# Optimization experiments

Hardware: AMD Instinct MI355X
Metric: run time of the kernel (lower is better)

Reference implementation:

```python
import jax, jax.numpy as jnp
import numpy as np

N = 40000   # number of points
K = 32      # neighbors per point (fixed-degree CSR for synthetic indices)
C = 256     # embed_dim
H = 8       # num_heads
HD = C // H # head_dim = 32
M = N * K   # number of (query, key) pairs


def setup_inputs() -> dict:
    key = jax.random.key(0)
    ks = jax.random.split(key, 12)
    s = 1.0 / np.sqrt(C).astype(np.float32)
    query_feats = jax.random.normal(ks[0], (N, C), jnp.float32)
    Wq = jax.random.normal(ks[1], (C, C), jnp.float32) * s
    bq = jax.random.normal(ks[2], (C,), jnp.float32) * 0.01
    Wk = jax.random.normal(ks[3], (C, C), jnp.float32) * s
    bk = jax.random.normal(ks[4], (C,), jnp.float32) * 0.01
    Wv = jax.random.normal(ks[5], (C, C), jnp.float32) * s
    bv = jax.random.normal(ks[6], (C,), jnp.float32) * 0.01
    Wp = jax.random.normal(ks[7], (C, C), jnp.float32) * s
    bp = jax.random.normal(ks[8], (C,), jnp.float32) * 0.01
    # CSR pair lists: index_0 sorted (K pairs per query point), index_1 = neighbor ids
    index_0 = jnp.repeat(jnp.arange(N, dtype=jnp.int32), K)
    index_1 = jax.random.randint(ks[9], (M,), 0, N, dtype=jnp.int32)
    sort_idx = jax.random.permutation(ks[10], N).astype(jnp.int32)
    return dict(query_feats=query_feats, Wq=Wq, bq=bq, Wk=Wk, bk=bk, Wv=Wv, bv=bv,
                Wp=Wp, bp=bp, index_0=index_0, index_1=index_1, sort_idx=sort_idx)


def reference(query_feats, Wq, bq, Wk, bk, Wv, bv, Wp, bp, index_0, index_1, sort_idx):
    # pe_type='none', attntion_type='qkv', key=value=query (self-attention), dropout=0
    scale = HD ** -0.5
    q = ((query_feats @ Wq) + bq).reshape(N, H, HD) * scale
    k = ((query_feats @ Wk) + bk).reshape(N, H, HD)
    v = ((query_feats @ Wv) + bv).reshape(N, H, HD)
    # sort into window-contiguous order
    qs = q[sort_idx]
    ks_ = k[sort_idx]
    vs = v[sort_idx]
    # attention_step1: per-pair QK dot over head_dim -> (M, H)
    attn = jnp.einsum('mhd,mhd->mh', qs[index_0], ks_[index_1])
    # scatter_softmax_csr over variable-length neighbor segments (grouped by index_0)
    seg_max = jax.ops.segment_max(attn, index_0, num_segments=N, indices_are_sorted=True)
    e = jnp.exp(attn - seg_max[index_0])
    seg_sum = jax.ops.segment_sum(e, index_0, num_segments=N, indices_are_sorted=True)
    p = e / seg_sum[index_0]  # (M, H)
    # attention_step2: weighted value gather + segment reduce -> (N, H, HD)
    xs = jax.ops.segment_sum(p[:, :, None] * vs[index_1], index_0,
                             num_segments=N, indices_are_sorted=True)
    # scatter back to original order: out[sort_idx] = xs
    x = jnp.zeros((N, C), query_feats.dtype).at[sort_idx].set(xs.reshape(N, C))
    # output projection
    return x @ Wp + bp
```

## Files before the change

### kernel.cpp

```cpp
#include <hip/hip_runtime.h>
#include <hip/hip_bf16.h>

#define NPTS 40000
#define KNBR 32
#define CDIM 256
#define NH 8
#define HD 32

static constexpr float QK_SCALE = 0.17677669529663687f;

typedef __attribute__((ext_vector_type(8))) __bf16 bf16x8;
typedef __attribute__((ext_vector_type(4))) __bf16 bf16x4;
typedef __attribute__((ext_vector_type(4))) float f32x4;

static __device__ __forceinline__ unsigned short bfbits(float f) {
    __bf16 h = (__bf16)f;
    union { __bf16 b; unsigned short u; } c; c.b = h;
    return c.u;
}

__global__ __launch_bounds__(256) void wtr_kernel(
    const float* __restrict__ W0, const float* __restrict__ W1,
    const float* __restrict__ W2, const float* __restrict__ W3,
    __bf16* __restrict__ T0, __bf16* __restrict__ T1,
    __bf16* __restrict__ T2, __bf16* __restrict__ T3)
{
    __shared__ float tile[32][33];
    const float* Ws[4] = {W0, W1, W2, W3};
    __bf16* Ts[4] = {T0, T1, T2, T3};
    const float* W = Ws[blockIdx.z];
    __bf16* Wt = Ts[blockIdx.z];
    const int t = threadIdx.x;
    const int k0 = blockIdx.x * 32, n0 = blockIdx.y * 32;
    const int r = t >> 3, c4 = (t & 7) * 4;
    const float4 v = *reinterpret_cast<const float4*>(&W[(k0 + r) * CDIM + n0 + c4]);
    tile[r][c4 + 0] = v.x; tile[r][c4 + 1] = v.y;
    tile[r][c4 + 2] = v.z; tile[r][c4 + 3] = v.w;
    __syncthreads();
    __bf16 o[4];
    #pragma unroll
    for (int i = 0; i < 4; ++i) o[i] = (__bf16)tile[c4 + i][r];
    *reinterpret_cast<ulong1*>(&Wt[(n0 + r) * CDIM + k0 + c4]) =
        *reinterpret_cast<ulong1*>(o);
}

__global__ __launch_bounds__(256, 2) void qkv_kernel(
    const float* __restrict__ X, const int* __restrict__ sort_idx,
    const __bf16* __restrict__ WtQ, const __bf16* __restrict__ WtK, const __bf16* __restrict__ WtV,
    const float* __restrict__ bq, const float* __restrict__ bk, const float* __restrict__ bv,
    __bf16* __restrict__ qs, unsigned int* __restrict__ kvs)
{
    __shared__ __bf16 xb[32][272];
    const int t = threadIdx.x;
    const int row0 = blockIdx.x * 32;

    #pragma unroll 8
    for (int r = 0; r < 32; ++r) {
        const int src = sort_idx[row0 + r];
        xb[r][t] = (__bf16)X[(size_t)src * CDIM + t];
    }
    __syncthreads();

    const int w = t >> 6, l = t & 63;
    const int lr = l & 15;
    const int lk = (l >> 4) * 8;
    const int nbase = w * 64;
    const __bf16* Wts[3] = {WtQ, WtK, WtV};

    f32x4 acc[3][2][4];
    #pragma unroll
    for (int s = 0; s < 3; ++s)
        #pragma unroll
        for (int mf = 0; mf < 2; ++mf)
            #pragma unroll
            for (int nf = 0; nf < 4; ++nf)
                acc[s][mf][nf] = (f32x4){0.f, 0.f, 0.f, 0.f};

    #pragma unroll 2
    for (int k0 = 0; k0 < CDIM; k0 += 32) {
        const bf16x8 a0 = *reinterpret_cast<const bf16x8*>(&xb[lr][k0 + lk]);
        const bf16x8 a1 = *reinterpret_cast<const bf16x8*>(&xb[16 + lr][k0 + lk]);
        #pragma unroll
        for (int s = 0; s < 3; ++s) {
            #pragma unroll
            for (int nf = 0; nf < 4; ++nf) {
                const bf16x8 b = *reinterpret_cast<const bf16x8*>(
                    Wts[s] + (size_t)(nbase + nf * 16 + lr) * CDIM + k0 + lk);
                acc[s][0][nf] = __builtin_amdgcn_mfma_f32_16x16x32_bf16(a0, b, acc[s][0][nf], 0, 0, 0);
                acc[s][1][nf] = __builtin_amdgcn_mfma_f32_16x16x32_bf16(a1, b, acc[s][1][nf], 0, 0, 0);
            }
        }
    }

    const int rbase = (l >> 4) * 4;
    #pragma unroll
    for (int nf = 0; nf < 4; ++nf) {
        const int col = nbase + nf * 16 + lr;
        const float bqv = bq[col], bkv = bk[col], bvv = bv[col];
        #pragma unroll
        for (int mf = 0; mf < 2; ++mf) {
            #pragma unroll
            for (int i = 0; i < 4; ++i) {
                const int row = row0 + mf * 16 + rbase + i;
                qs[row * CDIM + col] = (__bf16)((acc[0][mf][nf][i] + bqv) * QK_SCALE);
                const unsigned int kb = bfbits(acc[1][mf][nf][i] + bkv);
                const unsigned int vb = bfbits(acc[2][mf][nf][i] + bvv);
                kvs[row * CDIM + col] = kb | (vb << 16);
            }
        }
    }
}

__global__ __launch_bounds__(256, 8) void attn_kernel(
    const __bf16* __restrict__ qs, const unsigned int* __restrict__ kvs,
    const int* __restrict__ index_1, const int* __restrict__ sort_idx,
    __bf16* __restrict__ xbuf)
{
    const int wv = __builtin_amdgcn_readfirstlane(threadIdx.x) >> 6;
    const int n = blockIdx.x * 4 + wv;
    const int l = threadIdx.x & 63;
    const int c0 = l * 4;

    const bf16x4 qv4 = *reinterpret_cast<const bf16x4*>(&qs[(size_t)n * CDIM + c0]);
    const float qx = (float)qv4[0], qy = (float)qv4[1];
    const float qz = (float)qv4[2], qw = (float)qv4[3];
    float lsum = 0.f;
    float o0 = 0.f, o1 = 0.f, o2 = 0.f, o3 = 0.f;
    const int* idx = index_1 + (size_t)n * KNBR;

    #pragma unroll 4
    for (int j = 0; j < KNBR; ++j) {
        const int nb = idx[j];
        const uint4 kv = *reinterpret_cast<const uint4*>(&kvs[(size_t)nb * CDIM + c0]);
        const float k0 = __uint_as_float(kv.x << 16);
        const float v0 = __uint_as_float(kv.x & 0xffff0000u);
        const float k1 = __uint_as_float(kv.y << 16);
        const float v1 = __uint_as_float(kv.y & 0xffff0000u);
        const float k2 = __uint_as_float(kv.z << 16);
        const float v2 = __uint_as_float(kv.z & 0xffff0000u);
        const float k3 = __uint_as_float(kv.w << 16);
        const float v3 = __uint_as_float(kv.w & 0xffff0000u);
        float dot = qx * k0;
        dot = fmaf(qy, k1, dot);
        dot = fmaf(qz, k2, dot);
        dot = fmaf(qw, k3, dot);
        dot += __shfl_xor(dot, 1);
        dot += __shfl_xor(dot, 2);
        dot += __shfl_xor(dot, 4);
        const float e = __expf(dot);
        lsum += e;
        o0 = fmaf(e, v0, o0);
        o1 = fmaf(e, v1, o1);
        o2 = fmaf(e, v2, o2);
        o3 = fmaf(e, v3, o3);
    }

    const float inv = 1.f / lsum;
    const int orig = sort_idx[n];
    __bf16 o[4];
    o[0] = (__bf16)(o0 * inv); o[1] = (__bf16)(o1 * inv);
    o[2] = (__bf16)(o2 * inv); o[3] = (__bf16)(o3 * inv);
    *reinterpret_cast<ulong1*>(&xbuf[(size_t)orig * CDIM + c0]) =
        *reinterpret_cast<ulong1*>(o);
}

__global__ __launch_bounds__(256, 2) void proj_kernel(
    const __bf16* __restrict__ X, const __bf16* __restrict__ WtP, const float* __restrict__ bp,
    float* __restrict__ out)
{
    const int t = threadIdx.x;
    const int w = t >> 6, l = t & 63;
    const int row0 = blockIdx.x * 32;
    const int lr = l & 15;
    const int lk = (l >> 4) * 8;
    const int nbase = w * 64;

    const __bf16* pA0 = X + (size_t)(row0 + lr) * CDIM + lk;
    const __bf16* pA1 = X + (size_t)(row0 + 16 + lr) * CDIM + lk;

    f32x4 acc[2][4];
    #pragma unroll
    for (int mf = 0; mf < 2; ++mf)
        #pragma unroll
        for (int nf = 0; nf < 4; ++nf)
            acc[mf][nf] = (f32x4){0.f, 0.f, 0.f, 0.f};

    #pragma unroll 2
    for (int k0 = 0; k0 < CDIM; k0 += 32) {
        const bf16x8 a0 = *reinterpret_cast<const bf16x8*>(pA0 + k0);
        const bf16x8 a1 = *reinterpret_cast<const bf16x8*>(pA1 + k0);
        #pragma unroll
        for (int nf = 0; nf < 4; ++nf) {
            const bf16x8 b = *reinterpret_cast<const bf16x8*>(
                WtP + (size_t)(nbase + nf * 16 + lr) * CDIM + k0 + lk);
            acc[0][nf] = __builtin_amdgcn_mfma_f32_16x16x32_bf16(a0, b, acc[0][nf], 0, 0, 0);
            acc[1][nf] = __builtin_amdgcn_mfma_f32_16x16x32_bf16(a1, b, acc[1][nf], 0, 0, 0);
        }
    }

    const int rbase = (l >> 4) * 4;
    #pragma unroll
    for (int nf = 0; nf < 4; ++nf) {
        const int col = nbase + nf * 16 + lr;
        const float bpv = bp[col];
        #pragma unroll
        for (int mf = 0; mf < 2; ++mf) {
            #pragma unroll
            for (int i = 0; i < 4; ++i) {
                const int row = row0 + mf * 16 + rbase + i;
                out[row * CDIM + col] = acc[mf][nf][i] + bpv;
            }
        }
    }
}

extern "C" void kernel_launch(void* const* d_in, const int* in_sizes, int n_in,
                              void* d_out, int out_size, void* d_ws, size_t ws_size,
                              hipStream_t stream) {
    const float* qf  = (const float*)d_in[0];
    const float* Wq  = (const float*)d_in[1];
    const float* bq  = (const float*)d_in[2];
    const float* Wk  = (const float*)d_in[3];
    const float* bk  = (const float*)d_in[4];
    const float* Wv  = (const float*)d_in[5];
    const float* bv  = (const float*)d_in[6];
    const float* Wp  = (const float*)d_in[7];
    const float* bp  = (const float*)d_in[8];
    const int* index_1  = (const int*)d_in[10];
    const int* sort_idx = (const int*)d_in[11];
    float* out = (float*)d_out;

    __bf16* qs = (__bf16*)d_ws;
    unsigned int* kvs = (unsigned int*)(qs + (size_t)NPTS * CDIM);
    __bf16* xbuf = (__bf16*)(kvs + (size_t)NPTS * CDIM);
    __bf16* WtQ = xbuf + (size_t)NPTS * CDIM;
    __bf16* WtK = WtQ + CDIM * CDIM;
    __bf16* WtV = WtK + CDIM * CDIM;
    __bf16* WtP = WtV + CDIM * CDIM;

    wtr_kernel<<<dim3(8, 8, 4), 256, 0, stream>>>(Wq, Wk, Wv, Wp, WtQ, WtK, WtV, WtP);
    qkv_kernel<<<NPTS / 32, 256, 0, stream>>>(qf, sort_idx, WtQ, WtK, WtV, bq, bk, bv, qs, kvs);
    attn_kernel<<<NPTS / 4, 256, 0, stream>>>(qs, kvs, index_1, sort_idx, xbuf);
    proj_kernel<<<NPTS / 32, 256, 0, stream>>>(xbuf, WtP, bp, out);
}
```

Before: 289.0 us.

## Split K/V buffers, sort neighbor indices, and enlarge GEMM row tiles

Stores K and V in separate bf16 arrays instead of an interleaved packed buffer, so the attention kernel issues two 8-byte gathers per neighbor. Each wave loads its 32 neighbor indices once and bitonic-sorts them in registers, then broadcasts them with shuffles, aiming for better cache locality on the gathers. The QKV and projection GEMMs now use 64-row tiles, processing Q, K and V one after another to reuse the A fragments across more MFMAs. The risks are more memory transactions per neighbor, the cost of the sort network, and higher register pressure in the larger GEMM tiles.

Result: slower. 321.5 us (+11.3%).

```diff
diff --git a/kernel.cpp b/kernel.cpp
--- a/kernel.cpp
+++ b/kernel.cpp
@@ -12,12 +12,6 @@
 typedef __attribute__((ext_vector_type(8))) __bf16 bf16x8;
 typedef __attribute__((ext_vector_type(4))) __bf16 bf16x4;
 typedef __attribute__((ext_vector_type(4))) float f32x4;
-
-static __device__ __forceinline__ unsigned short bfbits(float f) {
-    __bf16 h = (__bf16)f;
-    union { __bf16 b; unsigned short u; } c; c.b = h;
-    return c.u;
-}
 
 __global__ __launch_bounds__(256) void wtr_kernel(
     const float* __restrict__ W0, const float* __restrict__ W1,
@@ -48,14 +42,14 @@
     const float* __restrict__ X, const int* __restrict__ sort_idx,
     const __bf16* __restrict__ WtQ, const __bf16* __restrict__ WtK, const __bf16* __restrict__ WtV,
     const float* __restrict__ bq, const float* __restrict__ bk, const float* __restrict__ bv,
-    __bf16* __restrict__ qs, unsigned int* __restrict__ kvs)
-{
-    __shared__ __bf16 xb[32][272];
+    __bf16* __restrict__ qs, __bf16* __restrict__ ksp, __bf16* __restrict__ vsp)
+{
+    __shared__ __bf16 xb[64][272];
     const int t = threadIdx.x;
-    const int row0 = blockIdx.x * 32;
+    const int row0 = blockIdx.x * 64;
 
     #pragma unroll 8
-    for (int r = 0; r < 32; ++r) {
+    for (int r = 0; r < 64; ++r) {
         const int src = sort_idx[row0 + r];
         xb[r][t] = (__bf16)X[(size_t)src * CDIM + t];
     }
@@ -65,54 +59,56 @@
     const int lr = l & 15;
     const int lk = (l >> 4) * 8;
     const int nbase = w * 64;
+    const int rbase = (l >> 4) * 4;
     const __bf16* Wts[3] = {WtQ, WtK, WtV};
-
-    f32x4 acc[3][2][4];
-    #pragma unroll
-    for (int s = 0; s < 3; ++s)
-        #pragma unroll
-        for (int mf = 0; mf < 2; ++mf)
+    const float* bias[3] = {bq, bk, bv};
+    __bf16* outs[3] = {qs, ksp, vsp};
+
+    #pragma unroll
+    for (int s = 0; s < 3; ++s) {
+        f32x4 acc[4][4];
+        #pragma unroll
+        for (int mf = 0; mf < 4; ++mf)
             #pragma unroll
             for (int nf = 0; nf < 4; ++nf)
-                acc[s][mf][nf] = (f32x4){0.f, 0.f, 0.f, 0.f};
-
-    #pragma unroll 2
-    for (int k0 = 0; k0 < CDIM; k0 += 32) {
-        const bf16x8 a0 = *reinterpret_cast<const bf16x8*>(&xb[lr][k0 + lk]);
-        const bf16x8 a1 = *reinterpret_cast<const bf16x8*>(&xb[16 + lr][k0 + lk]);
-        #pragma unroll
-        for (int s = 0; s < 3; ++s) {
+                acc[mf][nf] = (f32x4){0.f, 0.f, 0.f, 0.f};
+
+        #pragma unroll 2
+        for (int k0 = 0; k0 < CDIM; k0 += 32) {
+            bf16x8 a[4];
+            #pragma unroll
+            for (int mf = 0; mf < 4; ++mf)
+                a[mf] = *reinterpret_cast<const bf16x8*>(&xb[mf * 16 + lr][k0 + lk]);
             #pragma unroll
             for (int nf = 0; nf < 4; ++nf) {
                 const bf16x8 b = *reinterpret_cast<const bf16x8*>(
                     Wts[s] + (size_t)(nbase + nf * 16 + lr) * CDIM + k0 + lk);
-                acc[s][0][nf] = __builtin_amdgcn_mfma_f32_16x16x32_bf16(a0, b, acc[s][0][nf], 0, 0, 0);
-                acc[s][1][nf] = __builtin_amdgcn_mfma_f32_16x16x32_bf16(a1, b, acc[s][1][nf], 0, 0, 0);
+                #pragma unroll
+                for (int mf = 0; mf < 4; ++mf)
+                    acc[mf][nf] = __builtin_amdgcn_mfma_f32_16x16x32_bf16(a[mf], b, acc[mf][nf], 0, 0, 0);
             }
         }
-    }
-
-    const int rbase = (l >> 4) * 4;
-    #pragma unroll
-    for (int nf = 0; nf < 4; ++nf) {
-        const int col = nbase + nf * 16 + lr;
-        const float bqv = bq[col], bkv = bk[col], bvv = bv[col];
-        #pragma unroll
-        for (int mf = 0; mf < 2; ++mf) {
-            #pragma unroll
-            for (int i = 0; i < 4; ++i) {
-                const int row = row0 + mf * 16 + rbase + i;
-                qs[row * CDIM + col] = (__bf16)((acc[0][mf][nf][i] + bqv) * QK_SCALE);
-                const unsigned int kb = bfbits(acc[1][mf][nf][i] + bkv);
-                const unsigned int vb = bfbits(acc[2][mf][nf][i] + bvv);
-                kvs[row * CDIM + col] = kb | (vb << 16);
+
+        __bf16* const dst = outs[s];
+        #pragma unroll
+        for (int nf = 0; nf < 4; ++nf) {
+            const int col = nbase + nf * 16 + lr;
+            const float bb = bias[s][col];
+            #pragma unroll
+            for (int mf = 0; mf < 4; ++mf) {
+                #pragma unroll
+                for (int i = 0; i < 4; ++i) {
+                    const int row = row0 + mf * 16 + rbase + i;
+                    const float val = acc[mf][nf][i] + bb;
+                    dst[(size_t)row * CDIM + col] = (__bf16)(s == 0 ? val * QK_SCALE : val);
+                }
             }
         }
     }
 }
 
 __global__ __launch_bounds__(256, 8) void attn_kernel(
-    const __bf16* __restrict__ qs, const unsigned int* __restrict__ kvs,
+    const __bf16* __restrict__ qs, const __bf16* __restrict__ ksp, const __bf16* __restrict__ vsp,
     const int* __restrict__ index_1, const int* __restrict__ sort_idx,
     __bf16* __restrict__ xbuf)
 {
@@ -120,26 +116,37 @@
     const int n = blockIdx.x * 4 + wv;
     const int l = threadIdx.x & 63;
     const int c0 = l * 4;
+
+    int key = index_1[(size_t)n * KNBR + (l & 31)];
+    #pragma unroll
+    for (int k = 2; k <= 32; k <<= 1) {
+        #pragma unroll
+        for (int s = k >> 1; s > 0; s >>= 1) {
+            const int ll = l & 31;
+            const int other = __shfl_xor(key, s);
+            const bool asc = (ll & k) == 0;
+            const bool lower = (ll & s) == 0;
+            const int mn = key < other ? key : other;
+            const int mx = key < other ? other : key;
+            key = (asc == lower) ? mn : mx;
+        }
+    }
 
     const bf16x4 qv4 = *reinterpret_cast<const bf16x4*>(&qs[(size_t)n * CDIM + c0]);
     const float qx = (float)qv4[0], qy = (float)qv4[1];
     const float qz = (float)qv4[2], qw = (float)qv4[3];
     float lsum = 0.f;
     float o0 = 0.f, o1 = 0.f, o2 = 0.f, o3 = 0.f;
-    const int* idx = index_1 + (size_t)n * KNBR;
-
-    #pragma unroll 4
+
+    #pragma unroll
     for (int j = 0; j < KNBR; ++j) {
-        const int nb = idx[j];
-        const uint4 kv = *reinterpret_cast<const uint4*>(&kvs[(size_t)nb * CDIM + c0]);
-        const float k0 = __uint_as_float(kv.x << 16);
-        const float v0 = __uint_as_float(kv.x & 0xffff0000u);
-        const float k1 = __uint_as_float(kv.y << 16);
-        const float v1 = __uint_as_float(kv.y & 0xffff0000u);
-        const float k2 = __uint_as_float(kv.z << 16);
-        const float v2 = __uint_as_float(kv.z & 0xffff0000u);
-        const float k3 = __uint_as_float(kv.w << 16);
-        const float v3 = __uint_as_float(kv.w & 0xffff0000u);
+        const int nb = __shfl(key, j);
+        const uint2 kk = *reinterpret_cast<const uint2*>(&ksp[(size_t)nb * CDIM + c0]);
+        const uint2 vv = *reinterpret_cast<const uint2*>(&vsp[(size_t)nb * CDIM + c0]);
+        const float k0 = __uint_as_float(kk.x << 16);
+        const float k1 = __uint_as_float(kk.x & 0xffff0000u);
+        const float k2 = __uint_as_float(kk.y << 16);
+        const float k3 = __uint_as_float(kk.y & 0xffff0000u);
         float dot = qx * k0;
         dot = fmaf(qy, k1, dot);
         dot = fmaf(qz, k2, dot);
@@ -148,6 +155,10 @@
         dot += __shfl_xor(dot, 2);
         dot += __shfl_xor(dot, 4);
         const float e = __expf(dot);
+        const float v0 = __uint_as_float(vv.x << 16);
+        const float v1 = __uint_as_float(vv.x & 0xffff0000u);
+        const float v2 = __uint_as_float(vv.y << 16);
+        const float v3 = __uint_as_float(vv.y & 0xffff0000u);
         lsum += e;
         o0 = fmaf(e, v0, o0);
         o1 = fmaf(e, v1, o1);
@@ -170,45 +181,50 @@
 {
     const int t = threadIdx.x;
     const int w = t >> 6, l = t & 63;
-    const int row0 = blockIdx.x * 32;
+    const int row0 = blockIdx.x * 64;
     const int lr = l & 15;
     const int lk = (l >> 4) * 8;
     const int nbase = w * 64;
-
-    const __bf16* pA0 = X + (size_t)(row0 + lr) * CDIM + lk;
-    const __bf16* pA1 = X + (size_t)(row0 + 16 + lr) * CDIM + lk;
-
-    f32x4 acc[2][4];
-    #pragma unroll
-    for (int mf = 0; mf < 2; ++mf)
+    const int rbase = (l >> 4) * 4;
+
+    const __bf16* pA[4];
+    #pragma unroll
+    for (int mf = 0; mf < 4; ++mf)
+        pA[mf] = X + (size_t)(row0 + mf * 16 + lr) * CDIM + lk;
+
+    f32x4 acc[4][4];
+    #pragma unroll
+    for (int mf = 0; mf < 4; ++mf)
         #pragma unroll
         for (int nf = 0; nf < 4; ++nf)
             acc[mf][nf] = (f32x4){0.f, 0.f, 0.f, 0.f};
 
     #pragma unroll 2
     for (int k0 = 0; k0 < CDIM; k0 += 32) {
-        const bf16x8 a0 = *reinterpret_cast<const bf16x8*>(pA0 + k0);
-        const bf16x8 a1 = *reinterpret_cast<const bf16x8*>(pA1 + k0);
+        bf16x8 a[4];
+        #pragma unroll
+        for (int mf = 0; mf < 4; ++mf)
+            a[mf] = *reinterpret_cast<const bf16x8*>(pA[mf] + k0);
         #pragma unroll
         for (int nf = 0; nf < 4; ++nf) {
             const bf16x8 b = *reinterpret_cast<const bf16x8*>(
                 WtP + (size_t)(nbase + nf * 16 + lr) * CDIM + k0 + lk);
-            acc[0][nf] = __builtin_amdgcn_mfma_f32_16x16x32_bf16(a0, b, acc[0][nf], 0, 0, 0);
-            acc[1][nf] = __builtin_amdgcn_mfma_f32_16x16x32_bf16(a1, b, acc[1][nf], 0, 0, 0);
-        }
-    }
-
-    const int rbase = (l >> 4) * 4;
+            #pragma unroll
+            for (int mf = 0; mf < 4; ++mf)
+                acc[mf][nf] = __builtin_amdgcn_mfma_f32_16x16x32_bf16(a[mf], b, acc[mf][nf], 0, 0, 0);
+        }
+    }
+
     #pragma unroll
     for (int nf = 0; nf < 4; ++nf) {
         const int col = nbase + nf * 16 + lr;
         const float bpv = bp[col];
         #pragma unroll
-        for (int mf = 0; mf < 2; ++mf) {
+        for (int mf = 0; mf < 4; ++mf) {
             #pragma unroll
             for (int i = 0; i < 4; ++i) {
                 const int row = row0 + mf * 16 + rbase + i;
-                out[row * CDIM + col] = acc[mf][nf][i] + bpv;
+                out[(size_t)row * CDIM + col] = acc[mf][nf][i] + bpv;
             }
         }
     }
@@ -230,16 +246,17 @@
     const int* sort_idx = (const int*)d_in[11];
     float* out = (float*)d_out;
 
-    __bf16* qs = (__bf16*)d_ws;
-    unsigned int* kvs = (unsigned int*)(qs + (size_t)NPTS * CDIM);
-    __bf16* xbuf = (__bf16*)(kvs + (size_t)NPTS * CDIM);
+    __bf16* qs  = (__bf16*)d_ws;
+    __bf16* ksp = qs  + (size_t)NPTS * CDIM;
+    __bf16* vsp = ksp + (size_t)NPTS * CDIM;
+    __bf16* xbuf = vsp + (size_t)NPTS * CDIM;
     __bf16* WtQ = xbuf + (size_t)NPTS * CDIM;
     __bf16* WtK = WtQ + CDIM * CDIM;
     __bf16* WtV = WtK + CDIM * CDIM;
     __bf16* WtP = WtV + CDIM * CDIM;
 
     wtr_kernel<<<dim3(8, 8, 4), 256, 0, stream>>>(Wq, Wk, Wv, Wp, WtQ, WtK, WtV, WtP);
-    qkv_kernel<<<NPTS / 32, 256, 0, stream>>>(qf, sort_idx, WtQ, WtK, WtV, bq, bk, bv, qs, kvs);
-    attn_kernel<<<NPTS / 4, 256, 0, stream>>>(qs, kvs, index_1, sort_idx, xbuf);
-    proj_kernel<<<NPTS / 32, 256, 0, stream>>>(xbuf, WtP, bp, out);
-}
+    qkv_kernel<<<NPTS / 64, 256, 0, stream>>>(qf, sort_idx, WtQ, WtK, WtV, bq, bk, bv, qs, ksp, vsp);
+    attn_kernel<<<NPTS / 4, 256, 0, stream>>>(qs, ksp, vsp, index_1, sort_idx, xbuf);
+    proj_kernel<<<NPTS / 64, 256, 0, stream>>>(xbuf, WtP, bp, out);
+}
```
